# Kernel tuning notes

Hardware: AMD Instinct MI355X
Metric: run time of the kernel (lower is better)

## Reference

```python
import jax, jax.numpy as jnp
from jax import lax
import numpy as np
import math

B, N, M, SIG, HID, NFEAT, OUT, H = 256, 512, 16, 256, 256, 3, 10, 256
ALPHA, BETA = 1.0, 0.5


def setup_inputs() -> dict:
    key = jax.random.key(0)
    ks = jax.random.split(key, 12)
    s_g = 1.0 / math.sqrt(HID)
    s_f = 1.0 / math.sqrt(SIG)
    return {
        "x": jax.random.normal(ks[0], (B, 1, H, H), jnp.float32),
        "unif": jax.random.uniform(ks[1], (B, N), jnp.float32),
        "z": jax.random.normal(ks[2], (B, N, 2), jnp.float32),
        "m_g_params": jax.random.normal(ks[3], (1, 6 * M), jnp.float32),
        "gc1_w": jax.random.uniform(ks[4], (NFEAT, HID), jnp.float32, -s_g, s_g),
        "gc1_b": jax.random.uniform(ks[5], (HID,), jnp.float32, -s_g, s_g),
        "gc2_w": jax.random.uniform(ks[6], (HID, HID), jnp.float32, -s_g, s_g),
        "gc2_b": jax.random.uniform(ks[7], (HID,), jnp.float32, -s_g, s_g),
        "collapser1": 0.1 * jax.random.normal(ks[8], (SIG, N), jnp.float32),
        "collapser2": 0.1 * jax.random.normal(ks[9], (SIG, N), jnp.float32),
        "fcf_w": jax.random.uniform(ks[10], (OUT, SIG), jnp.float32, -s_f, s_f),
        "fcf_b": jax.random.uniform(ks[11], (OUT,), jnp.float32, -s_f, s_f),
    }


def _mixture_fields(m_g_params):
    # torch: split [num_sample, 6M] into M chunks of 6, stack -> [M, N, 6],
    # split along last dim, then .view(N, M) in C-order on the [M, N] field.
    raw = m_g_params.reshape(M, 6)  # [M, 6]
    return [jnp.broadcast_to(raw[:, j][:, None], (M, N)).reshape(N, M) for j in range(6)]


def reference(x, unif, z, m_g_params, gc1_w, gc1_b, gc2_w, gc2_b,
              collapser1, collapser2, fcf_w, fcf_b):
    pi_f, mux_f, muy_f, sx_f, sy_f, rho_f = _mixture_fields(m_g_params)
    pi = jax.nn.softmax(pi_f, axis=-1)            # [N, M]
    # categorical sampling via CDF inversion, vectorized over batch
    cdf = jnp.cumsum(pi, axis=-1)                 # [N, M]
    idx = jnp.argmax(unif[:, :, None] < cdf[None], axis=-1)  # [B, N]
    row = jnp.arange(N)[None, :]
    gat = lambda f: f[row, idx]                   # [B, N]
    mux, muy = gat(mux_f), gat(muy_f)
    sx, sy = jnp.exp(gat(sx_f)), jnp.exp(gat(sy_f))
    rho = jnp.tanh(gat(rho_f))
    # reparameterized bivariate-normal sample via Cholesky (lower)
    z1, z2 = z[..., 0], z[..., 1]
    xs = mux + sx * z1
    ys = muy + sy * (rho * z1 + jnp.sqrt(1.0 - rho * rho) * z2)
    # torch MVN.sample() is no_grad -> detach samples
    xs_c, ys_c = lax.stop_gradient(xs), lax.stop_gradient(ys)
    dx, dy = xs_c - mux, ys_c - muy
    omr2 = 1.0 - rho * rho
    quad = (dx * dx / (sx * sx) - 2.0 * rho * dx * dy / (sx * sy) + dy * dy / (sy * sy)) / omr2
    logprob = (-jnp.log(2.0 * jnp.pi) - jnp.log(sx * sy)
               - 0.5 * jnp.log(omr2) - 0.5 * quad)  # [B, N]
    full_log_prob = logprob.sum(axis=-1)           # [B]
    loc = jnp.tanh(jnp.stack([xs_c, ys_c], axis=-1))  # [B, N, 2]
    # adjacency: inverse shifted pairwise squared distance
    diff = loc[:, :, None, :] - loc[:, None, :, :]  # [B, N, N, 2]
    adj = 1.0 / (ALPHA + BETA * jnp.sum(diff * diff, axis=-1))  # [B, N, N]
    # pixel gather: denormalize (trunc toward zero, like torch .long())
    pix = jnp.trunc(0.5 * (loc + 1.0) * H - 0.1).astype(jnp.int32)
    pix = jnp.clip(pix, 0, H - 1)
    bidx = jnp.arange(B)[:, None]
    pv = x[bidx, :, pix[..., 0], pix[..., 1]]      # [B, N, 1]
    feat = jnp.concatenate([pv, loc], axis=-1)     # [B, N, 3]
    # GCN (eval mode: no dropout)
    s1 = jax.nn.relu(jnp.einsum('bnm,bmh->bnh', adj, feat @ gc1_w) + gc1_b)
    s2 = jax.nn.relu(jnp.einsum('bnm,bmh->bnh', adj, s1 @ gc2_w) + gc2_b)
    # nn.Softmax() (no dim) on 3D input resolves to dim=0 in torch
    g1 = jax.nn.softmax(jnp.einsum('sn,bnh->bsh', collapser1, s1), axis=0)
    g2 = jax.nn.softmax(jnp.einsum('sn,bnh->bsh', collapser2, s2), axis=0)
    sig = (g1 + g2).sum(axis=2)                    # [B, SIG]
    out = jax.nn.softmax(sig @ fcf_w.T + fcf_b, axis=-1)  # [B, OUT]
    return out, full_log_prob
```

## Files before the change

### kernel.cpp

```cpp
#include <hip/hip_runtime.h>
#include <hip/hip_bf16.h>
#include <math.h>

#define Bx   256
#define Nx   512
#define SIGx 256
#define HIDx 256
#define OUTx 10
#define Hx   256

typedef __attribute__((ext_vector_type(4))) float f32x4;
typedef long fp8x8;
typedef unsigned char uchar;

__device__ inline uchar f2fp8(float v) {
    int r = __builtin_amdgcn_cvt_pk_fp8_f32(v, 0.0f, 0, false);
    return (uchar)(r & 0xff);
}
__device__ inline uint pk4fp8(float a0, float a1, float a2, float a3) {
    int r = __builtin_amdgcn_cvt_pk_fp8_f32(a0, a1, 0, false);
    r = __builtin_amdgcn_cvt_pk_fp8_f32(a2, a3, r, true);
    return (uint)r;
}

__global__ __launch_bounds__(512) void kA_sample(
    const float* __restrict__ x, const float* __restrict__ z,
    const float* __restrict__ mg, float* __restrict__ feat,
    float* __restrict__ flp)
{
    int b = blockIdx.x;
    int n = threadIdx.x;
    int g = n >> 5;
    float mux = mg[g*6+1];
    float muy = mg[g*6+2];
    float sxv = expf(mg[g*6+3]);
    float syv = expf(mg[g*6+4]);
    float rho = tanhf(mg[g*6+5]);
    float z1 = z[((size_t)b*Nx + n)*2 + 0];
    float z2 = z[((size_t)b*Nx + n)*2 + 1];
    float omr2 = 1.0f - rho*rho;
    float xs = mux + sxv*z1;
    float ys = muy + syv*(rho*z1 + sqrtf(omr2)*z2);
    float dx = xs - mux, dy = ys - muy;
    float quad = (dx*dx/(sxv*sxv) - 2.0f*rho*dx*dy/(sxv*syv) + dy*dy/(syv*syv)) / omr2;
    float logprob = -1.8378770664093453f - logf(sxv*syv) - 0.5f*logf(omr2) - 0.5f*quad;
    float lx = tanhf(xs), ly = tanhf(ys);
    int px = (int)truncf(0.5f*(lx+1.0f)*(float)Hx - 0.1f);
    int py = (int)truncf(0.5f*(ly+1.0f)*(float)Hx - 0.1f);
    px = px < 0 ? 0 : (px > Hx-1 ? Hx-1 : px);
    py = py < 0 ? 0 : (py > Hx-1 ? Hx-1 : py);
    float pv = x[(size_t)b*Hx*Hx + (size_t)px*Hx + py];
    size_t fo = ((size_t)b*Nx + n)*3;
    feat[fo+0] = pv; feat[fo+1] = lx; feat[fo+2] = ly;

    __shared__ float red[512];
    red[n] = logprob;
    __syncthreads();
    for (int st = 256; st > 0; st >>= 1) {
        if (n < st) red[n] += red[n+st];
        __syncthreads();
    }
    if (n == 0) flp[b] = red[0];
}

__global__ __launch_bounds__(256) void kPrep(
    const float* __restrict__ c1, const float* __restrict__ c2,
    const float* __restrict__ w2,
    uchar* __restrict__ c1q, uchar* __restrict__ c2q, uchar* __restrict__ w2tq)
{
    int idx = blockIdx.x*256 + threadIdx.x;
    if (idx < SIGx*Nx) {
        c1q[idx] = f2fp8(16.0f * c1[idx]);
        c2q[idx] = f2fp8(16.0f * c2[idx]);
    }
    if (idx < HIDx*HIDx) {
        int i = idx >> 8, j = idx & 255;
        w2tq[idx] = f2fp8(16.0f * w2[j*HIDx + i]);
    }
}

__global__ __launch_bounds__(512) void kFuse1(
    const float* __restrict__ featL, const float* __restrict__ w1,
    const float* __restrict__ b1,
    uchar* __restrict__ adjAll, uchar* __restrict__ s1tAll)
{
    int b = blockIdx.x;
    const float* fb = featL + (size_t)b*Nx*3;
    uchar* adj = adjAll + (size_t)b*Nx*Nx;
    uchar* s1t = s1tAll + (size_t)b*HIDx*Nx;

    __shared__ float fpv[Nx], flx[Nx], fly[Nx], fH[Nx];
    __shared__ float w1s[3*HIDx], b1s[HIDx];
    __shared__ float Gp[4][3][Nx];

    int t = threadIdx.x;
    {
        float pv = fb[t*3+0], lx = fb[t*3+1], ly = fb[t*3+2];
        fpv[t] = pv; flx[t] = lx; fly[t] = ly;
        fH[t] = fmaf(0.5f*lx, lx, fmaf(0.5f*ly, ly, 1.0f));
    }
    for (int i = t; i < 3*HIDx; i += 512) w1s[i] = w1[i];
    if (t < HIDx) b1s[t] = b1[t];
    __syncthreads();

    int tq = t & 127;
    int mc = t >> 7;
    int n4 = tq*4;

    float xn[4], yn[4], cn[4];
    #pragma unroll
    for (int e = 0; e < 4; ++e) {
        xn[e] = flx[n4+e]; yn[e] = fly[n4+e];
        cn[e] = fmaf(0.5f*xn[e], xn[e], 0.5f*yn[e]*yn[e]);
    }
    float G0[4] = {}, G1[4] = {}, G2[4] = {};

    int m0 = mc*128;
    #pragma unroll 4
    for (int mm = 0; mm < 128; ++mm) {
        int m = m0 + mm;
        float hx = fH[m], fx = flx[m], fy = fly[m];
        float a[4];
        #pragma unroll
        for (int e = 0; e < 4; ++e) {
            float s = fmaf(-yn[e], fy, fmaf(-xn[e], fx, hx + cn[e]));
            a[e] = __builtin_amdgcn_rcpf(s);
            G0[e] = fmaf(a[e], fpv[m], G0[e]);
            G1[e] = fmaf(a[e], fx, G1[e]);
            G2[e] = fmaf(a[e], fy, G2[e]);
        }
        *(uint*)(adj + (size_t)m*Nx + n4) = pk4fp8(a[0], a[1], a[2], a[3]);
    }

    *(f32x4*)&Gp[mc][0][n4] = (f32x4){G0[0],G0[1],G0[2],G0[3]};
    *(f32x4*)&Gp[mc][1][n4] = (f32x4){G1[0],G1[1],G1[2],G1[3]};
    *(f32x4*)&Gp[mc][2][n4] = (f32x4){G2[0],G2[1],G2[2],G2[3]};
    __syncthreads();

    f32x4 T0 = {}, T1 = {}, T2 = {};
    #pragma unroll
    for (int j = 0; j < 4; ++j) {
        T0 += *(const f32x4*)&Gp[j][0][n4];
        T1 += *(const f32x4*)&Gp[j][1][n4];
        T2 += *(const f32x4*)&Gp[j][2][n4];
    }

    int hc = mc;
    #pragma unroll 4
    for (int hh = 0; hh < 64; ++hh) {
        int h = hc*64 + hh;
        float w0 = w1s[h], wA = w1s[HIDx+h], wB = w1s[2*HIDx+h], bb = b1s[h];
        float v0 = fminf(fmaxf(fmaf(T0.x,w0, fmaf(T1.x,wA, fmaf(T2.x,wB, bb))), 0.0f), 448.0f);
        float v1 = fminf(fmaxf(fmaf(T0.y,w0, fmaf(T1.y,wA, fmaf(T2.y,wB, bb))), 0.0f), 448.0f);
        float v2 = fminf(fmaxf(fmaf(T0.z,w0, fmaf(T1.z,wA, fmaf(T2.z,wB, bb))), 0.0f), 448.0f);
        float v3 = fminf(fmaxf(fmaf(T0.w,w0, fmaf(T1.w,wA, fmaf(T2.w,wB, bb))), 0.0f), 448.0f);
        *(uint*)(s1t + (size_t)h*Nx + n4) = pk4fp8(v0, v1, v2, v3);
    }
}

__global__ __launch_bounds__(256) void kGemmAdjQ(
    const uchar* __restrict__ Aall, const uchar* __restrict__ adjAll,
    const float* __restrict__ bias, uchar* __restrict__ outAll)
{
    int b    = blockIdx.x;
    int tile = blockIdx.y;
    int rt = tile >> 2;
    int ct = tile & 3;
    const uchar* A = Aall + (size_t)b*HIDx*Nx;
    const uchar* Badj = adjAll + (size_t)b*Nx*Nx;
    uchar* outp = outAll + (size_t)b*HIDx*Nx;

    __shared__ uchar Als[128][80];
    __shared__ uchar Bls[128][80];
    int t = threadIdx.x;
    int lane = t & 63, wave = t >> 6;
    int wr = wave >> 1, wc = wave & 1;
    int q = lane >> 4, c16 = lane & 15;
    int r0 = rt*128, n0 = ct*128;
    f32x4 acc[4][4] = {};

    for (int kk = 0; kk < Nx; kk += 64) {
        #pragma unroll
        for (int cc = 0; cc < 2; ++cc) {
            int c = t + cc*256;
            int row = c >> 2;
            int ko = (c & 3) * 16;
            *(float4*)&Als[row][ko] = *(const float4*)(A + (size_t)(r0+row)*Nx + kk + ko);
            *(float4*)&Bls[row][ko] = *(const float4*)(Badj + (size_t)(n0+row)*Nx + kk + ko);
        }
        __syncthreads();
        #pragma unroll
        for (int ks = 0; ks < 64; ks += 32) {
            fp8x8 af[4], bfr[4];
            #pragma unroll
            for (int i = 0; i < 4; ++i)
                af[i] = *(const fp8x8*)&Als[wr*64 + i*16 + c16][ks + q*8];
            #pragma unroll
            for (int j = 0; j < 4; ++j)
                bfr[j] = *(const fp8x8*)&Bls[wc*64 + j*16 + c16][ks + q*8];
            #pragma unroll
            for (int i = 0; i < 4; ++i)
                #pragma unroll
                for (int j = 0; j < 4; ++j)
                    acc[i][j] = __builtin_amdgcn_mfma_f32_16x16x32_fp8_fp8(af[i], bfr[j], acc[i][j], 0, 0, 0);
        }
        __syncthreads();
    }
    #pragma unroll
    for (int i = 0; i < 4; ++i) {
        int rowb = r0 + wr*64 + i*16 + q*4;
        #pragma unroll
        for (int j = 0; j < 4; ++j) {
            int col = n0 + wc*64 + j*16 + c16;
            #pragma unroll
            for (int r = 0; r < 4; ++r) {
                float v = fmaxf(acc[i][j][r] + bias[rowb + r], 0.0f) * 0.25f;
                outp[(size_t)(rowb + r)*Nx + col] = f2fp8(fminf(v, 448.0f));
            }
        }
    }
}

template<int K, int NC, bool TRB>
__global__ __launch_bounds__(256) void kGstdQ(
    const uchar* __restrict__ Ash, const uchar* __restrict__ Ball,
    uchar* __restrict__ outAll, float oscale)
{
    constexpr int CT = NC / 128;
    int b    = blockIdx.x;
    int tile = blockIdx.y;
    int rt = tile / CT;
    int ct = tile % CT;
    const uchar* B = Ball + (size_t)b*HIDx*Nx;
    uchar* outp = outAll + (size_t)b*HIDx*NC;

    __shared__ uchar Als[128][80];
    __shared__ uchar Bls[128][80];
    int t = threadIdx.x;
    int lane = t & 63, wave = t >> 6;
    int wr = wave >> 1, wc = wave & 1;
    int q = lane >> 4, c16 = lane & 15;
    int r0 = rt*128, n0 = ct*128;
    f32x4 acc[4][4] = {};

    for (int kk = 0; kk < K; kk += 64) {
        #pragma unroll
        for (int cc = 0; cc < 2; ++cc) {
            int c = t + cc*256;
            int row = c >> 2;
            int ko = (c & 3) * 16;
            *(float4*)&Als[row][ko] = *(const float4*)(Ash + (size_t)(r0+row)*K + kk + ko);
        }
        if (!TRB) {
            #pragma unroll
            for (int cc = 0; cc < 2; ++cc) {
                int c = t + cc*256;
                int row = c >> 2;
                int ko = (c & 3) * 16;
                *(float4*)&Bls[row][ko] = *(const float4*)(B + (size_t)(n0+row)*K + kk + ko);
            }
        } else {
            int pi  = t & 31;
            int nc8 = t >> 5;
            int hk = kk + 2*pi;
            const uchar* g0 = B + (size_t)hk*NC + n0 + nc8*16;
            const uchar* g1 = g0 + NC;
            float4 v0 = *(const float4*)g0;
            float4 v1 = *(const float4*)g1;
            const uchar* pa = (const uchar*)&v0;
            const uchar* qa = (const uchar*)&v1;
            #pragma unroll
            for (int e = 0; e < 16; ++e)
                *(ushort*)&Bls[nc8*16 + e][2*pi] = (ushort)pa[e] | ((ushort)qa[e] << 8);
        }
        __syncthreads();
        #pragma unroll
        for (int ks = 0; ks < 64; ks += 32) {
            fp8x8 af[4], bfr[4];
            #pragma unroll
            for (int i = 0; i < 4; ++i)
                af[i] = *(const fp8x8*)&Als[wr*64 + i*16 + c16][ks + q*8];
            #pragma unroll
            for (int j = 0; j < 4; ++j)
                bfr[j] = *(const fp8x8*)&Bls[wc*64 + j*16 + c16][ks + q*8];
            #pragma unroll
            for (int i = 0; i < 4; ++i)
                #pragma unroll
                for (int j = 0; j < 4; ++j)
                    acc[i][j] = __builtin_amdgcn_mfma_f32_16x16x32_fp8_fp8(af[i], bfr[j], acc[i][j], 0, 0, 0);
        }
        __syncthreads();
    }
    #pragma unroll
    for (int i = 0; i < 4; ++i) {
        int rowb = r0 + wr*64 + i*16 + q*4;
        #pragma unroll
        for (int j = 0; j < 4; ++j) {
            int col = n0 + wc*64 + j*16 + c16;
            #pragma unroll
            for (int r = 0; r < 4; ++r) {
                float v = acc[i][j][r] * oscale;
                v = fminf(fmaxf(v, -448.0f), 448.0f);
                outp[(size_t)(rowb + r)*NC + col] = f2fp8(v);
            }
        }
    }
}

__global__ __launch_bounds__(512) void kF1q(
    const uchar* __restrict__ t1, const uchar* __restrict__ t2,
    float* __restrict__ m1, float* __restrict__ rd1,
    float* __restrict__ m2, float* __restrict__ rd2)
{
    int s = blockIdx.x;
    int t = threadIdx.x;
    int hq = t & 63;
    int bq = t >> 6;
    const size_t str = (size_t)SIGx*HIDx;
    size_t base = (size_t)(bq*32)*str + (size_t)s*HIDx + hq*4;

    float mv1[4], dv1[4], mv2[4], dv2[4];
    #pragma unroll
    for (int e = 0; e < 4; ++e) { mv1[e]=-3.0e38f; dv1[e]=0.0f; mv2[e]=-3.0e38f; dv2[e]=0.0f; }

    for (int i = 0; i < 32; ++i) {
        uint u1 = *(const uint*)(t1 + base + (size_t)i*str);
        uint u2 = *(const uint*)(t2 + base + (size_t)i*str);
        float v1[4], v2[4];
        v1[0] = __builtin_amdgcn_cvt_f32_fp8(u1, 0);
        v1[1] = __builtin_amdgcn_cvt_f32_fp8(u1, 1);
        v1[2] = __builtin_amdgcn_cvt_f32_fp8(u1, 2);
        v1[3] = __builtin_amdgcn_cvt_f32_fp8(u1, 3);
        v2[0] = __builtin_amdgcn_cvt_f32_fp8(u2, 0);
        v2[1] = __builtin_amdgcn_cvt_f32_fp8(u2, 1);
        v2[2] = __builtin_amdgcn_cvt_f32_fp8(u2, 2);
        v2[3] = __builtin_amdgcn_cvt_f32_fp8(u2, 3);
        #pragma unroll
        for (int e = 0; e < 4; ++e) {
            float mn;
            mn = fmaxf(mv1[e], v1[e]);
            dv1[e] = dv1[e]*__expf(mv1[e]-mn) + __expf(v1[e]-mn); mv1[e] = mn;
            mn = fmaxf(mv2[e], v2[e]);
            dv2[e] = dv2[e]*__expf(mv2[e]-mn) + __expf(v2[e]-mn); mv2[e] = mn;
        }
    }

    __shared__ float pm1[8][256], pd1[8][256], pm2[8][256], pd2[8][256];
    #pragma unroll
    for (int e = 0; e < 4; ++e) {
        pm1[bq][hq*4+e] = mv1[e]; pd1[bq][hq*4+e] = dv1[e];
        pm2[bq][hq*4+e] = mv2[e]; pd2[bq][hq*4+e] = dv2[e];
    }
    __syncthreads();

    if (t < 256) {
        int h = t;
        float m = -3.0e38f, d = 0.0f;
        #pragma unroll
        for (int j = 0; j < 8; ++j) {
            float mm = pm1[j][h], dd = pd1[j][h];
            float mn = fmaxf(m, mm);
            d = d*__expf(m-mn) + dd*__expf(mm-mn);
            m = mn;
        }
        size_t o = (size_t)s*HIDx + h;
        m1[o] = m; rd1[o] = 1.0f/d;
    } else {
        int h = t - 256;
        float m = -3.0e38f, d = 0.0f;
        #pragma unroll
        for (int j = 0; j < 8; ++j) {
            float mm = pm2[j][h], dd = pd2[j][h];
            float mn = fmaxf(m, mm);
            d = d*__expf(m-mn) + dd*__expf(mm-mn);
            m = mn;
        }
        size_t o = (size_t)s*HIDx + h;
        m2[o] = m; rd2[o] = 1.0f/d;
    }
}

__global__ __launch_bounds__(256) void kF2q(
    const uchar* __restrict__ t1, const uchar* __restrict__ t2,
    const float* __restrict__ m1, const float* __restrict__ rd1,
    const float* __restrict__ m2, const float* __restrict__ rd2,
    float* __restrict__ sig)
{
    int b = blockIdx.y;
    int sq = threadIdx.x >> 6;
    int s = blockIdx.x*4 + sq;
    int hq = threadIdx.x & 63;
    size_t sh = (size_t)s*HIDx + hq*4;
    size_t tb = ((size_t)b*SIGx + s)*HIDx + hq*4;
    uint u1 = *(const uint*)(t1 + tb);
    uint u2 = *(const uint*)(t2 + tb);
    f32x4 a1 = *(const f32x4*)&m1[sh];
    f32x4 r1 = *(const f32x4*)&rd1[sh];
    f32x4 a2 = *(const f32x4*)&m2[sh];
    f32x4 r2 = *(const f32x4*)&rd2[sh];
    float v = 0.0f;
    v += __expf(__builtin_amdgcn_cvt_f32_fp8(u1,0) - a1.x) * r1.x;
    v += __expf(__builtin_amdgcn_cvt_f32_fp8(u1,1) - a1.y) * r1.y;
    v += __expf(__builtin_amdgcn_cvt_f32_fp8(u1,2) - a1.z) * r1.z;
    v += __expf(__builtin_amdgcn_cvt_f32_fp8(u1,3) - a1.w) * r1.w;
    v += __expf(__builtin_amdgcn_cvt_f32_fp8(u2,0) - a2.x) * r2.x;
    v += __expf(__builtin_amdgcn_cvt_f32_fp8(u2,1) - a2.y) * r2.y;
    v += __expf(__builtin_amdgcn_cvt_f32_fp8(u2,2) - a2.z) * r2.z;
    v += __expf(__builtin_amdgcn_cvt_f32_fp8(u2,3) - a2.w) * r2.w;

    __shared__ float red[256];
    red[threadIdx.x] = v;
    __syncthreads();
    for (int st = 32; st > 0; st >>= 1) {
        if (hq < st) red[threadIdx.x] += red[threadIdx.x + st];
        __syncthreads();
    }
    if (hq == 0) sig[(size_t)b*SIGx + s] = red[sq*64];
}

__global__ __launch_bounds__(256) void kG_out(
    const float* __restrict__ sig, const float* __restrict__ fw,
    const float* __restrict__ fb, float* __restrict__ out)
{
    int b = blockIdx.x;
    int tid = threadIdx.x;
    __shared__ float red[256];
    __shared__ float logits[OUTx];
    float sv = sig[(size_t)b*SIGx + tid];
    for (int o = 0; o < OUTx; ++o) {
        red[tid] = sv * fw[o*SIGx + tid];
        __syncthreads();
        for (int st = 128; st > 0; st >>= 1) {
            if (tid < st) red[tid] += red[tid+st];
            __syncthreads();
        }
        if (tid == 0) logits[o] = red[0] + fb[o];
        __syncthreads();
    }
    if (tid == 0) {
        float mx = logits[0];
        for (int o = 1; o < OUTx; ++o) mx = fmaxf(mx, logits[o]);
        float dd = 0.0f; float e[OUTx];
        for (int o = 0; o < OUTx; ++o) { e[o] = expf(logits[o]-mx); dd += e[o]; }
        float inv = 1.0f/dd;
        for (int o = 0; o < OUTx; ++o) out[(size_t)b*OUTx + o] = e[o]*inv;
    }
}

static inline size_t alignup(size_t b) { return (b + 255) & ~(size_t)255; }

extern "C" void kernel_launch(void* const* d_in, const int* in_sizes, int n_in,
                              void* d_out, int out_size, void* d_ws, size_t ws_size,
                              hipStream_t stream)
{
    const float* x   = (const float*)d_in[0];
    const float* z   = (const float*)d_in[2];
    const float* mg  = (const float*)d_in[3];
    const float* w1  = (const float*)d_in[4];
    const float* b1  = (const float*)d_in[5];
    const float* w2  = (const float*)d_in[6];
    const float* b2  = (const float*)d_in[7];
    const float* c1  = (const float*)d_in[8];
    const float* c2  = (const float*)d_in[9];
    const float* fw  = (const float*)d_in[10];
    const float* fbv = (const float*)d_in[11];
    float* out = (float*)d_out;
    float* flp = out + (size_t)Bx*OUTx;
    (void)in_sizes; (void)n_in; (void)out_size;

    char* ws = (char*)d_ws;
    size_t off = 0;
    auto alloc = [&](size_t bytes) -> char* {
        char* p = ws + off; off += alignup(bytes); return p;
    };
    float*  feat = (float*)alloc((size_t)Bx*Nx*3*4);
    uchar*  c1q  = (uchar*)alloc((size_t)SIGx*Nx);
    uchar*  c2q  = (uchar*)alloc((size_t)SIGx*Nx);
    uchar*  w2tq = (uchar*)alloc((size_t)HIDx*HIDx);
    uchar*  t1   = (uchar*)alloc((size_t)Bx*SIGx*HIDx);
    uchar*  t2   = (uchar*)alloc((size_t)Bx*SIGx*HIDx);
    float*  m1   = (float*)alloc((size_t)SIGx*HIDx*4);
    float*  d1   = (float*)alloc((size_t)SIGx*HIDx*4);
    float*  m2   = (float*)alloc((size_t)SIGx*HIDx*4);
    float*  d2   = (float*)alloc((size_t)SIGx*HIDx*4);
    float*  sig  = (float*)alloc((size_t)Bx*SIGx*4);
    size_t fixed = off;

    int BC = 1;
    for (int c = Bx; c >= 1; c >>= 1) {
        size_t need = fixed + alignup((size_t)c*Nx*Nx)
                            + 2*alignup((size_t)c*HIDx*Nx);
        if (need <= ws_size) { BC = c; break; }
    }
    uchar* Padj = (uchar*)alloc((size_t)BC*Nx*Nx);
    uchar* P1   = (uchar*)alloc((size_t)BC*HIDx*Nx);
    uchar* P2   = (uchar*)alloc((size_t)BC*HIDx*Nx);

    hipLaunchKernelGGL(kA_sample, dim3(Bx), dim3(Nx), 0, stream, x, z, mg, feat, flp);
    hipLaunchKernelGGL(kPrep, dim3(512), dim3(256), 0, stream, c1, c2, w2, c1q, c2q, w2tq);

    const int nch = Bx / BC;
    for (int c = 0; c < nch; ++c) {
        int b0 = c * BC;
        const float* featL = feat + (size_t)b0*Nx*3;
        uchar* t1L = t1 + (size_t)b0*SIGx*HIDx;
        uchar* t2L = t2 + (size_t)b0*SIGx*HIDx;
        hipLaunchKernelGGL(kFuse1, dim3(BC), dim3(512), 0, stream,
                           featL, w1, b1, Padj, P2);
        hipLaunchKernelGGL((kGstdQ<512,256,false>), dim3(BC, 4), dim3(256), 0, stream,
                           c1q, P2, t1L, 0.0625f);
        hipLaunchKernelGGL((kGstdQ<256,512,true>), dim3(BC, 8), dim3(256), 0, stream,
                           w2tq, P2, P1, 0.0625f);
        hipLaunchKernelGGL(kGemmAdjQ, dim3(BC, 8), dim3(256), 0, stream, P1, Padj, b2, P2);
        hipLaunchKernelGGL((kGstdQ<512,256,false>), dim3(BC, 4), dim3(256), 0, stream,
                           c2q, P2, t2L, 0.25f);
    }

    hipLaunchKernelGGL(kF1q, dim3(SIGx), dim3(512), 0, stream,
                       t1, t2, m1, d1, m2, d2);
    hipLaunchKernelGGL(kF2q, dim3(SIGx/4, Bx), dim3(256), 0, stream,
                       t1, t2, m1, d1, m2, d2, sig);
    hipLaunchKernelGGL(kG_out, dim3(Bx), dim3(256), 0, stream, sig, fw, fbv, out);
}
```

Before: 316.6 us.

## Load GEMM tiles directly to LDS with XOR-swizzled unpadded layout

Replaces the register-staged global-to-shared copies in the fp8 MFMA GEMM kernels with global_load_lds direct-to-LDS transfers. The shared tiles lose their padding and switch to an XOR-swizzled 64-byte row layout, so fragment reads avoid bank conflicts and the copy instructions write contiguous 1 KB chunks per wave. The transposed-B path keeps register staging but writes into the same swizzled layout. This cuts VGPR traffic and load/store instruction count during tile staging. It relies on the swizzle being applied consistently on the load and read sides.

Result: faster. 291.4 us (-8.0%).

```diff
diff --git a/kernel.cpp b/kernel.cpp
--- a/kernel.cpp
+++ b/kernel.cpp
@@ -21,6 +21,16 @@
     int r = __builtin_amdgcn_cvt_pk_fp8_f32(a0, a1, 0, false);
     r = __builtin_amdgcn_cvt_pk_fp8_f32(a2, a3, r, true);
     return (uint)r;
+}
+
+__device__ inline void gload_lds16(const uchar* g, uchar* l) {
+    __builtin_amdgcn_global_load_lds(
+        (const __attribute__((address_space(1))) uint*)g,
+        (__attribute__((address_space(3))) uint*)l, 16, 0, 0);
+}
+__device__ inline const uchar* laddr(const uchar* base, int row, int kb) {
+    int ps = (kb >> 4) ^ ((row >> 1) & 3) ^ ((row >> 4) & 3);
+    return base + row*64 + ps*16 + (kb & 15);
 }
 
 __global__ __launch_bounds__(512) void kA_sample(
@@ -170,23 +180,25 @@
     const uchar* Badj = adjAll + (size_t)b*Nx*Nx;
     uchar* outp = outAll + (size_t)b*HIDx*Nx;
 
-    __shared__ uchar Als[128][80];
-    __shared__ uchar Bls[128][80];
+    __shared__ __align__(16) uchar Als[128*64];
+    __shared__ __align__(16) uchar Bls[128*64];
     int t = threadIdx.x;
     int lane = t & 63, wave = t >> 6;
     int wr = wave >> 1, wc = wave & 1;
     int q = lane >> 4, c16 = lane & 15;
     int r0 = rt*128, n0 = ct*128;
+    int lrow = lane >> 2;
+    int pu   = lane & 3;
     f32x4 acc[4][4] = {};
 
     for (int kk = 0; kk < Nx; kk += 64) {
         #pragma unroll
-        for (int cc = 0; cc < 2; ++cc) {
-            int c = t + cc*256;
-            int row = c >> 2;
-            int ko = (c & 3) * 16;
-            *(float4*)&Als[row][ko] = *(const float4*)(A + (size_t)(r0+row)*Nx + kk + ko);
-            *(float4*)&Bls[row][ko] = *(const float4*)(Badj + (size_t)(n0+row)*Nx + kk + ko);
+        for (int r = 0; r < 2; ++r) {
+            int chunk = wave*2 + r;
+            int row = chunk*16 + lrow;
+            int sl = pu ^ ((row>>1)&3) ^ ((row>>4)&3);
+            gload_lds16(A + (size_t)(r0+row)*Nx + kk + sl*16, Als + chunk*1024);
+            gload_lds16(Badj + (size_t)(n0+row)*Nx + kk + sl*16, Bls + chunk*1024);
         }
         __syncthreads();
         #pragma unroll
@@ -194,10 +206,10 @@
             fp8x8 af[4], bfr[4];
             #pragma unroll
             for (int i = 0; i < 4; ++i)
-                af[i] = *(const fp8x8*)&Als[wr*64 + i*16 + c16][ks + q*8];
+                af[i] = *(const fp8x8*)laddr(Als, wr*64 + i*16 + c16, ks + q*8);
             #pragma unroll
             for (int j = 0; j < 4; ++j)
-                bfr[j] = *(const fp8x8*)&Bls[wc*64 + j*16 + c16][ks + q*8];
+                bfr[j] = *(const fp8x8*)laddr(Bls, wc*64 + j*16 + c16, ks + q*8);
             #pragma unroll
             for (int i = 0; i < 4; ++i)
                 #pragma unroll
@@ -234,32 +246,28 @@
     const uchar* B = Ball + (size_t)b*HIDx*Nx;
     uchar* outp = outAll + (size_t)b*HIDx*NC;
 
-    __shared__ uchar Als[128][80];
-    __shared__ uchar Bls[128][80];
+    __shared__ __align__(16) uchar Als[128*64];
+    __shared__ __align__(16) uchar Bls[128*64];
     int t = threadIdx.x;
     int lane = t & 63, wave = t >> 6;
     int wr = wave >> 1, wc = wave & 1;
     int q = lane >> 4, c16 = lane & 15;
     int r0 = rt*128, n0 = ct*128;
+    int lrow = lane >> 2;
+    int pu   = lane & 3;
     f32x4 acc[4][4] = {};
 
     for (int kk = 0; kk < K; kk += 64) {
         #pragma unroll
-        for (int cc = 0; cc < 2; ++cc) {
-            int c = t + cc*256;
-            int row = c >> 2;
-            int ko = (c & 3) * 16;
-            *(float4*)&Als[row][ko] = *(const float4*)(Ash + (size_t)(r0+row)*K + kk + ko);
-        }
-        if (!TRB) {
-            #pragma unroll
-            for (int cc = 0; cc < 2; ++cc) {
-                int c = t + cc*256;
-                int row = c >> 2;
-                int ko = (c & 3) * 16;
-                *(float4*)&Bls[row][ko] = *(const float4*)(B + (size_t)(n0+row)*K + kk + ko);
-            }
-        } else {
+        for (int r = 0; r < 2; ++r) {
+            int chunk = wave*2 + r;
+            int row = chunk*16 + lrow;
+            int sl = pu ^ ((row>>1)&3) ^ ((row>>4)&3);
+            gload_lds16(Ash + (size_t)(r0+row)*K + kk + sl*16, Als + chunk*1024);
+            if (!TRB)
+                gload_lds16(B + (size_t)(n0+row)*K + kk + sl*16, Bls + chunk*1024);
+        }
+        if (TRB) {
             int pi  = t & 31;
             int nc8 = t >> 5;
             int hk = kk + 2*pi;
@@ -269,9 +277,15 @@
             float4 v1 = *(const float4*)g1;
             const uchar* pa = (const uchar*)&v0;
             const uchar* qa = (const uchar*)&v1;
-            #pragma unroll
-            for (int e = 0; e < 16; ++e)
-                *(ushort*)&Bls[nc8*16 + e][2*pi] = (ushort)pa[e] | ((ushort)qa[e] << 8);
+            int kb = 2*pi;
+            int s  = kb >> 4;
+            #pragma unroll
+            for (int e = 0; e < 16; ++e) {
+                int row = nc8*16 + e;
+                int ps = s ^ ((row>>1)&3) ^ ((row>>4)&3);
+                *(ushort*)(Bls + row*64 + ps*16 + (kb & 15)) =
+                    (ushort)pa[e] | ((ushort)qa[e] << 8);
+            }
         }
         __syncthreads();
         #pragma unroll
@@ -279,10 +293,10 @@
             fp8x8 af[4], bfr[4];
             #pragma unroll
             for (int i = 0; i < 4; ++i)
-                af[i] = *(const fp8x8*)&Als[wr*64 + i*16 + c16][ks + q*8];
+                af[i] = *(const fp8x8*)laddr(Als, wr*64 + i*16 + c16, ks + q*8);
             #pragma unroll
             for (int j = 0; j < 4; ++j)
-                bfr[j] = *(const fp8x8*)&Bls[wc*64 + j*16 + c16][ks + q*8];
+                bfr[j] = *(const fp8x8*)laddr(Bls, wc*64 + j*16 + c16, ks + q*8);
             #pragma unroll
             for (int i = 0; i < 4; ++i)
                 #pragma unroll
```
